# Kernel tuning notes

Hardware: AMD Instinct MI355X
Metric: run time of the kernel (lower is better)

## Reference

```python
import jax, jax.numpy as jnp
import numpy as np

H = 8      # heads
D = 64     # dim_head
DIM = 512  # model dim (== H*D)
LN_EPS = 1e-5


def setup_inputs() -> dict:
    key = jax.random.key(0)
    ks = jax.random.split(key, 4)
    B, N = 8, 1024
    x = jax.random.normal(ks[0], (B, N, DIM), dtype=jnp.float32)
    # params (torch Linear y = x @ W^T; we store W already transposed as (in, out))
    w_qkv = jax.random.normal(ks[1], (DIM, 3 * H * D), dtype=jnp.float32) * (DIM ** -0.5)
    w_out = jax.random.normal(ks[2], (H * D, DIM), dtype=jnp.float32) * ((H * D) ** -0.5)
    b_out = jnp.zeros((DIM,), dtype=jnp.float32)
    ln_g = jnp.ones((DIM,), dtype=jnp.float32)
    ln_b = jnp.zeros((DIM,), dtype=jnp.float32)
    return {"x": x, "w_qkv": w_qkv, "w_out": w_out, "b_out": b_out,
            "ln_g": ln_g, "ln_b": ln_b}


def reference(x, w_qkv, w_out, b_out, ln_g, ln_b):
    b, n, _ = x.shape
    qkv = x @ w_qkv                                   # [b, n, 3*H*D]
    q, k, v = jnp.split(qkv, 3, axis=-1)              # each [b, n, H*D]

    def to_heads(t):                                  # 'b n (h d) -> (b h) n d'
        return t.reshape(b, n, H, D).transpose(0, 2, 1, 3).reshape(b * H, n, D)

    q = to_heads(q)
    k = to_heads(k)
    v = to_heads(v)

    # FAITHFUL to source: k.view(b*h, -1, n) is a row-major reshape, NOT a
    # transpose, and NO scale is applied (self.scale is unused in forward).
    k_r = k.reshape(b * H, D, n)                      # [(bh), D, n] reinterpreted
    dots = jnp.matmul(q, k_r)                          # [(bh), n, n]
    attn = jax.nn.softmax(dots, axis=-1)
    out = jnp.matmul(attn, v)                          # [(bh), n, D]

    # '(b h) n d -> b n (h d)'
    out = out.reshape(b, H, n, D).transpose(0, 2, 1, 3).reshape(b, n, H * D)
    out = out @ w_out + b_out                          # to_out Linear (dropout=0)

    mu = jnp.mean(out, axis=-1, keepdims=True)
    var = jnp.var(out, axis=-1, keepdims=True)
    out = (out - mu) * jax.lax.rsqrt(var + LN_EPS) * ln_g + ln_b
    return out + x
```

## Files before the change

kernel.cpp:

```cpp
#include <hip/hip_runtime.h>

typedef unsigned short u16;
typedef unsigned int u32;
typedef __attribute__((ext_vector_type(4))) float f32x4;
typedef __attribute__((ext_vector_type(8))) short s16x8;
typedef __attribute__((ext_vector_type(4))) unsigned int u32x4;

__device__ __forceinline__ u16 bf16_rne(float f) {
    u32 u = __float_as_uint(f);
    u32 r = u + 0x7FFFu + ((u >> 16) & 1u);
    return (u16)(r >> 16);
}

__device__ __forceinline__ u32 cvt_pk_bf16(float lo, float hi) {
    u32 r;
    asm("v_cvt_pk_bf16_f32 %0, %1, %2" : "=v"(r) : "v"(lo), "v"(hi));
    return r;
}

__device__ __forceinline__ void gl_lds16(const void* g, void* l) {
    __builtin_amdgcn_global_load_lds(
        (const __attribute__((address_space(1))) u32*)g,
        (__attribute__((address_space(3))) u32*)l, 16, 0, 0);
}

#define MFMA16(a, b, c) __builtin_amdgcn_mfma_f32_16x16x32_bf16((a), (b), (c), 0, 0, 0)

__global__ __launch_bounds__(256) void k_transpose2(const float* __restrict__ w_qkv,
                                                    const float* __restrict__ w_out,
                                                    u16* __restrict__ wqkvt,
                                                    u16* __restrict__ woutt) {
    __shared__ float tile[32][33];
    const float* in;
    u16* out;
    int C, bxc;
    if (blockIdx.x < 48) { in = w_qkv; out = wqkvt; C = 1536; bxc = blockIdx.x; }
    else                 { in = w_out; out = woutt; C = 512;  bxc = blockIdx.x - 48; }
    const int R = 512;
    int bx = bxc * 32;
    int by = blockIdx.y * 32;
    int tx = threadIdx.x;
    int ty = threadIdx.y;
#pragma unroll
    for (int i = 0; i < 32; i += 8)
        tile[ty + i][tx] = in[(size_t)(by + ty + i) * C + bx + tx];
    __syncthreads();
#pragma unroll
    for (int i = 0; i < 32; i += 8)
        out[(size_t)(bx + ty + i) * R + by + tx] = bf16_rne(tile[tx][ty + i]);
}

__global__ __launch_bounds__(256) void k_qkv_gemm(
    const float* __restrict__ x, const u16* __restrict__ wt,
    u16* __restrict__ qh, u16* __restrict__ kRT, u16* __restrict__ vT) {
    __shared__ __align__(16) u16 lA[2][128 * 64];
    __shared__ __align__(16) u16 lB[2][128 * 64];
    const int tid = threadIdx.x;
    const int lane = tid & 63, l15 = lane & 15, l4 = lane >> 4;
    const int wid = tid >> 6, wm = wid >> 1, wn = wid & 1;
    const int m0 = blockIdx.y * 128;
    const int c0 = blockIdx.x * 128;

    const char* gX = (const char*)x + (size_t)m0 * 2048;
    const char* gB = (const char*)wt + (size_t)c0 * 1024;
    const int srow = tid >> 3;
    const int cc = tid & 7;
    const int scol = cc * 16;

    const f32x4 z4 = {0.f, 0.f, 0.f, 0.f};
    f32x4 acc[4][4];
#pragma unroll
    for (int i = 0; i < 4; ++i)
#pragma unroll
        for (int j = 0; j < 4; ++j) acc[i][j] = z4;

    f32x4 ax[4][2];
    auto loadA = [&](int kt) {
#pragma unroll
        for (int q = 0; q < 4; ++q) {
            const char* src = gX + (size_t)(q * 32 + srow) * 2048 + kt * 256 + cc * 32;
            ax[q][0] = *(const f32x4*)(src);
            ax[q][1] = *(const f32x4*)(src + 16);
        }
    };
    auto writeA = [&](int buf) {
#pragma unroll
        for (int q = 0; q < 4; ++q) {
            int row = q * 32 + srow;
            u32x4 v;
            v.x = cvt_pk_bf16(ax[q][0].x, ax[q][0].y);
            v.y = cvt_pk_bf16(ax[q][0].z, ax[q][0].w);
            v.z = cvt_pk_bf16(ax[q][1].x, ax[q][1].y);
            v.w = cvt_pk_bf16(ax[q][1].z, ax[q][1].w);
            *(u32x4*)((char*)lA[buf] + row * 128 + (scol ^ ((row & 7) << 4))) = v;
        }
    };
    auto stageB = [&](int buf, int kt) {
#pragma unroll
        for (int q = 0; q < 4; ++q) {
            int row = q * 32 + srow;
            int sc = scol ^ ((row & 7) << 4);
            gl_lds16(gB + (size_t)row * 1024 + kt * 128 + sc,
                     (char*)lB[buf] + q * 4096 + tid * 16);
        }
    };

    loadA(0);
    stageB(0, 0);
    writeA(0);
    __syncthreads();
    for (int kt = 0; kt < 8; ++kt) {
        int buf = kt & 1;
        if (kt < 7) {
            loadA(kt + 1);
            stageB(buf ^ 1, kt + 1);
        }
        s16x8 af[4][2], bfr[4][2];
#pragma unroll
        for (int i = 0; i < 4; ++i)
#pragma unroll
            for (int k2 = 0; k2 < 2; ++k2) {
                int ra = wm * 64 + i * 16 + l15;
                int ca = (k2 * 64 + l4 * 16) ^ ((ra & 7) << 4);
                af[i][k2] = *(const s16x8*)((const char*)lA[buf] + ra * 128 + ca);
                int rb = wn * 64 + i * 16 + l15;
                int cb = (k2 * 64 + l4 * 16) ^ ((rb & 7) << 4);
                bfr[i][k2] = *(const s16x8*)((const char*)lB[buf] + rb * 128 + cb);
            }
        __builtin_amdgcn_s_setprio(1);
#pragma unroll
        for (int i = 0; i < 4; ++i)
#pragma unroll
            for (int j = 0; j < 4; ++j)
#pragma unroll
                for (int k2 = 0; k2 < 2; ++k2)
                    acc[i][j] = MFMA16(af[i][k2], bfr[j][k2], acc[i][j]);
        __builtin_amdgcn_s_setprio(0);
        if (kt < 7) writeA(buf ^ 1);
        __syncthreads();
    }

    char* ct = (char*)lA;
    const int which = c0 >> 9;
    const int hb = (c0 & 511) >> 6;
    const int b = m0 >> 10;
    const int n0 = m0 & 1023;
    const int i4 = (m0 >> 7) & 7;

    if (which != 2) {
#pragma unroll
        for (int i = 0; i < 4; ++i)
#pragma unroll
            for (int j = 0; j < 4; ++j) {
                int col = wn * 64 + j * 16 + l15;
#pragma unroll
                for (int r = 0; r < 4; ++r) {
                    int rr = wm * 64 + i * 16 + l4 * 4 + r;
                    *(u16*)(ct + rr * 256 + ((col * 2) ^ ((rr & 7) << 4))) =
                        bf16_rne(acc[i][j][r]);
                }
            }
    } else {
#pragma unroll
        for (int i = 0; i < 4; ++i)
#pragma unroll
            for (int j = 0; j < 4; ++j) {
                int col = wn * 64 + j * 16 + l15;
#pragma unroll
                for (int r = 0; r < 4; ++r) {
                    int rr = wm * 64 + i * 16 + l4 * 4 + r;
                    *(u16*)(ct + col * 256 + ((rr * 2) ^ ((col & 7) << 4))) =
                        bf16_rne(acc[i][j][r]);
                }
            }
    }
    __syncthreads();

    if (which == 0) {
#pragma unroll
        for (int p = 0; p < 8; ++p) {
            int cid = p * 256 + tid;
            int row = cid >> 4, sub = cid & 15;
            s16x8 v = *(const s16x8*)(ct + row * 256 + ((sub * 16) ^ ((row & 7) << 4)));
            int bh = b * 8 + hb + (sub >> 3);
            *(s16x8*)((char*)qh + ((size_t)bh * 1024 + n0 + row) * 128 +
                      (sub & 7) * 16) = v;
        }
    } else if (which == 1) {
#pragma unroll
        for (int p = 0; p < 8; ++p) {
            int cid = p * 256 + tid;
            int h = cid >> 10, jb = (cid >> 6) & 15, jd = cid & 63;
            int colb = ((h * 64 + jd) * 2) ^ ((jb & 7) << 4);
            s16x8 v;
#pragma unroll
            for (int ii = 0; ii < 8; ++ii)
                v[ii] = *(const short*)(ct + (jb + ii * 16) * 256 + colb);
            int bh = b * 8 + hb + h;
            *(s16x8*)((char*)kRT + (size_t)bh * 131072 + jb * 8192 + i4 * 1024 +
                      jd * 16) = v;
        }
    } else {
#pragma unroll
        for (int p = 0; p < 8; ++p) {
            int cid = p * 256 + tid;
            int cl = cid >> 4, nc = cid & 15;
            s16x8 v = *(const s16x8*)(ct + cl * 256 + ((nc * 16) ^ ((cl & 7) << 4)));
            int bh = b * 8 + hb + (cl >> 6);
            *(s16x8*)((char*)vT + ((size_t)bh * 64 + (cl & 63)) * 2048 + n0 * 2 +
                      nc * 16) = v;
        }
    }
}

__global__ __launch_bounds__(512) void k_attn(
    const u16* __restrict__ qh, const u16* __restrict__ kRT,
    const u16* __restrict__ vT, u16* __restrict__ attn_out) {
    __shared__ __align__(16) char smem[49152];
    char* qtile = smem;
    char* ktb = smem + 16384;
    char* vtb = smem + 32768;

    const int tid = threadIdx.x;
    const int lane = tid & 63, l15 = lane & 15, l4 = lane >> 4;
    const int wid = tid >> 6;
    const int bh = blockIdx.x, mt = blockIdx.y;

    const char* kb = (const char*)kRT + (size_t)bh * 131072;
    const char* vb = (const char*)vT + (size_t)bh * 64 * 2048;
    const int srow = tid >> 3;
    const int scol = (tid & 7) * 16;

    {
        const char* gq = (const char*)qh + ((size_t)bh * 1024 + mt * 128) * 128;
#pragma unroll
        for (int q = 0; q < 2; ++q) {
            int row = q * 64 + srow;
            int sc = scol ^ ((row & 7) << 4);
            gl_lds16(gq + (size_t)row * 128 + sc, qtile + q * 8192 + tid * 16);
        }
        int i4s = (tid & 7) ^ (srow & 7);
        gl_lds16(kb + i4s * 1024 + srow * 16, ktb + tid * 16);
        int sc = scol ^ ((srow & 7) << 4);
        gl_lds16(vb + (size_t)srow * 2048 + sc, vtb + tid * 16);
    }
    __syncthreads();

    s16x8 qf[2];
#pragma unroll
    for (int k2 = 0; k2 < 2; ++k2) {
        int row = wid * 16 + l15;
        int cq = (k2 * 64 + l4 * 16) ^ ((row & 7) << 4);
        qf[k2] = *(const s16x8*)(qtile + row * 128 + cq);
    }
    __syncthreads();

    char* ptw = smem + wid * 2048;

    const f32x4 z4 = {0.f, 0.f, 0.f, 0.f};
    f32x4 o[4];
    float den = 0.f;
#pragma unroll
    for (int d4 = 0; d4 < 4; ++d4) o[d4] = z4;
    const float LOG2E = 1.4426950408889634f;

    for (int jb = 0; jb < 16; ++jb) {
        const int buf = jb & 1;
        if (jb < 15) {
            int nb = jb + 1, bufn = buf ^ 1;
            int i4s = (tid & 7) ^ (srow & 7);
            gl_lds16(kb + (size_t)nb * 8192 + i4s * 1024 + srow * 16,
                     ktb + bufn * 8192 + tid * 16);
            int sc = scol ^ ((srow & 7) << 4);
            gl_lds16(vb + (size_t)srow * 2048 + nb * 128 + sc,
                     vtb + bufn * 8192 + tid * 16);
        }
        const char* kt = ktb + buf * 8192;
        const char* vt = vtb + buf * 8192;

        s16x8 bk[4][2];
#pragma unroll
        for (int n4 = 0; n4 < 4; ++n4)
#pragma unroll
            for (int k2 = 0; k2 < 2; ++k2) {
                int rn = n4 * 16 + l15;
                int cb = (k2 * 64 + l4 * 16) ^ ((rn & 7) << 4);
                bk[n4][k2] = *(const s16x8*)(kt + rn * 128 + cb);
            }
        f32x4 s[4];
        __builtin_amdgcn_s_setprio(1);
#pragma unroll
        for (int n4 = 0; n4 < 4; ++n4) {
            s[n4] = z4;
#pragma unroll
            for (int k2 = 0; k2 < 2; ++k2)
                s[n4] = MFMA16(bk[n4][k2], qf[k2], s[n4]);
        }
        __builtin_amdgcn_s_setprio(0);

#pragma unroll
        for (int n4 = 0; n4 < 4; ++n4) {
            float e0 = exp2f(s[n4][0] * LOG2E);
            float e1 = exp2f(s[n4][1] * LOG2E);
            float e2 = exp2f(s[n4][2] * LOG2E);
            float e3 = exp2f(s[n4][3] * LOG2E);
            den += (e0 + e1) + (e2 + e3);
            uint2 w;
            w.x = cvt_pk_bf16(e0, e1);
            w.y = cvt_pk_bf16(e2, e3);
            *(uint2*)(ptw + l15 * 128 +
                      ((n4 * 32 + l4 * 8) ^ ((l15 & 7) << 4))) = w;
        }

        s16x8 bv[4][2];
#pragma unroll
        for (int d4 = 0; d4 < 4; ++d4)
#pragma unroll
            for (int k2 = 0; k2 < 2; ++k2) {
                int rn = d4 * 16 + l15;
                int cb = (k2 * 64 + l4 * 16) ^ ((rn & 7) << 4);
                bv[d4][k2] = *(const s16x8*)(vt + rn * 128 + cb);
            }

        s16x8 pa[2];
#pragma unroll
        for (int k2 = 0; k2 < 2; ++k2)
            pa[k2] = *(const s16x8*)(ptw + l15 * 128 +
                                     ((k2 * 64 + l4 * 16) ^ ((l15 & 7) << 4)));

        __builtin_amdgcn_s_setprio(1);
#pragma unroll
        for (int d4 = 0; d4 < 4; ++d4)
#pragma unroll
            for (int k2 = 0; k2 < 2; ++k2)
                o[d4] = MFMA16(bv[d4][k2], pa[k2], o[d4]);
        __builtin_amdgcn_s_setprio(0);

        if (jb < 15) __syncthreads();
    }

    den += __shfl_xor(den, 16);
    den += __shfl_xor(den, 32);
    float inv = 1.0f / den;

    {
        int row = wid * 16 + l15;
        char* ow = smem + row * 128;
#pragma unroll
        for (int d4 = 0; d4 < 4; ++d4) {
            uint2 w;
            w.x = cvt_pk_bf16(o[d4][0] * inv, o[d4][1] * inv);
            w.y = cvt_pk_bf16(o[d4][2] * inv, o[d4][3] * inv);
            *(uint2*)(ow + ((d4 * 32 + l4 * 8) ^ ((row & 7) << 4))) = w;
        }
    }
    __syncthreads();

    {
        char* dst = (char*)attn_out + ((size_t)(bh >> 3) * 1024 + mt * 128) * 1024 +
                    (bh & 7) * 128;
#pragma unroll
        for (int p = 0; p < 2; ++p) {
            int cid = p * 512 + tid;
            int row = cid >> 3, sub = cid & 7;
            s16x8 v = *(const s16x8*)(smem + row * 128 +
                                      ((sub * 16) ^ ((row & 7) << 4)));
            *(s16x8*)(dst + (size_t)row * 1024 + sub * 16) = v;
        }
    }
}

__global__ __launch_bounds__(512) void k_out_ln(
    const u16* __restrict__ aout, const u16* __restrict__ wt,
    const float* __restrict__ bias, const float* __restrict__ x,
    const float* __restrict__ g, const float* __restrict__ bb,
    float* __restrict__ out) {
    __shared__ __align__(16) char smem[131072];
    char* lB[2] = {smem, smem + 65536};
    const int tid = threadIdx.x;
    const int lane = tid & 63, l15 = lane & 15, l4 = lane >> 4;
    const int wid = tid >> 6, wm = wid >> 2, wn = wid & 3;
    const int m0 = blockIdx.x * 32;

    s16x8 af[16];
    {
        const char* arow = (const char*)aout + (size_t)(m0 + wm * 16 + l15) * 1024;
#pragma unroll
        for (int kk = 0; kk < 16; ++kk)
            af[kk] = *(const s16x8*)(arow + kk * 64 + l4 * 16);
    }

    auto stageB = [&](int buf, int kt) {
#pragma unroll
        for (int p = 0; p < 8; ++p) {
            int cid = p * 512 + tid;
            int n = cid >> 3, cc = cid & 7;
            int sc = (cc * 16) ^ ((n & 7) << 4);
            gl_lds16((const char*)wt + (size_t)n * 1024 + kt * 128 + sc,
                     lB[buf] + cid * 16);
        }
    };

    const f32x4 z4 = {0.f, 0.f, 0.f, 0.f};
    f32x4 acc[8];
#pragma unroll
    for (int j = 0; j < 8; ++j) acc[j] = z4;

    stageB(0, 0);
    __syncthreads();
    for (int kt = 0; kt < 8; ++kt) {
        int buf = kt & 1;
        if (kt < 7) stageB(buf ^ 1, kt + 1);
        s16x8 bf2[8][2];
#pragma unroll
        for (int j = 0; j < 8; ++j)
#pragma unroll
            for (int q = 0; q < 2; ++q) {
                int n = wn * 128 + j * 16 + l15;
                int cb = (q * 64 + l4 * 16) ^ ((n & 7) << 4);
                bf2[j][q] = *(const s16x8*)(lB[buf] + n * 128 + cb);
            }
        __builtin_amdgcn_s_setprio(1);
#pragma unroll
        for (int j = 0; j < 8; ++j)
#pragma unroll
            for (int q = 0; q < 2; ++q)
                acc[j] = MFMA16(af[kt * 2 + q], bf2[j][q], acc[j]);
        __builtin_amdgcn_s_setprio(0);
        __syncthreads();
    }

#pragma unroll
    for (int j = 0; j < 8; ++j) {
        int col = wn * 128 + j * 16 + l15;
        float bo = bias[col];
#pragma unroll
        for (int r = 0; r < 4; ++r) {
            int row = wm * 16 + l4 * 4 + r;
            *(float*)(smem + row * 2048 + ((col * 4) ^ ((row & 7) << 4))) =
                acc[j][r] + bo;
        }
    }
    __syncthreads();

    f32x4 g0 = *(const f32x4*)(g + lane * 8);
    f32x4 g1 = *(const f32x4*)(g + lane * 8 + 4);
    f32x4 b0 = *(const f32x4*)(bb + lane * 8);
    f32x4 b1 = *(const f32x4*)(bb + lane * 8 + 4);
#pragma unroll
    for (int rr = 0; rr < 4; ++rr) {
        int row = wid * 4 + rr;
        int sw = (row & 7) << 4;
        f32x4 v0 = *(const f32x4*)(smem + row * 2048 + ((lane * 32) ^ sw));
        f32x4 v1 = *(const f32x4*)(smem + row * 2048 + ((lane * 32 + 16) ^ sw));
        float s = v0.x + v0.y + v0.z + v0.w + v1.x + v1.y + v1.z + v1.w;
        float sq = v0.x * v0.x + v0.y * v0.y + v0.z * v0.z + v0.w * v0.w +
                   v1.x * v1.x + v1.y * v1.y + v1.z * v1.z + v1.w * v1.w;
#pragma unroll
        for (int m = 1; m < 64; m <<= 1) {
            s += __shfl_xor(s, m);
            sq += __shfl_xor(sq, m);
        }
        float mu = s * (1.0f / 512.0f);
        float var = sq * (1.0f / 512.0f) - mu * mu;
        float rstd = rsqrtf(var + 1e-5f);

        const float* xr = x + (size_t)(m0 + row) * 512 + lane * 8;
        f32x4 x0 = *(const f32x4*)(xr);
        f32x4 x1 = *(const f32x4*)(xr + 4);
        f32x4 r0, r1;
#pragma unroll
        for (int u = 0; u < 4; ++u) {
            r0[u] = (v0[u] - mu) * rstd * g0[u] + b0[u] + x0[u];
            r1[u] = (v1[u] - mu) * rstd * g1[u] + b1[u] + x1[u];
        }
        float* orow = out + (size_t)(m0 + row) * 512 + lane * 8;
        *(f32x4*)(orow) = r0;
        *(f32x4*)(orow + 4) = r1;
    }
}

extern "C" void kernel_launch(void* const* d_in, const int* in_sizes, int n_in,
                              void* d_out, int out_size, void* d_ws, size_t ws_size,
                              hipStream_t stream) {
    const float* x = (const float*)d_in[0];
    const float* w_qkv = (const float*)d_in[1];
    const float* w_out = (const float*)d_in[2];
    const float* b_out = (const float*)d_in[3];
    const float* ln_g = (const float*)d_in[4];
    const float* ln_b = (const float*)d_in[5];
    float* out = (float*)d_out;
    char* ws = (char*)d_ws;

    u16* wqkvt = (u16*)(ws + 0);
    u16* woutt = (u16*)(ws + 1572864);
    u16* qh = (u16*)(ws + 2097152);
    u16* kRT = (u16*)(ws + 10485760);
    u16* vT = (u16*)(ws + 18874368);
    u16* aout = (u16*)(ws + 27262976);

    k_transpose2<<<dim3(64, 16), dim3(32, 8), 0, stream>>>(w_qkv, w_out, wqkvt, woutt);
    k_qkv_gemm<<<dim3(12, 64), 256, 0, stream>>>(x, wqkvt, qh, kRT, vT);
    k_attn<<<dim3(64, 8), 512, 0, stream>>>(qh, kRT, vT, aout);
    k_out_ln<<<256, 512, 0, stream>>>(aout, woutt, b_out, x, ln_g, ln_b, out);
}
```

Measured before the change: 87.46 us.

## Pre-convert x to bf16 and stage A via direct global-to-LDS loads with block swizzle

Adds a separate kernel that converts x from fp32 to bf16 once. The QKV GEMM can then stage its A operand through global_load_lds the same way as B, instead of loading fp32 into registers, converting, and writing to LDS. This removes the register pressure and the VALU conversion work inside the GEMM main loop, and it stops each of the 12 column tiles from re-reading and re-converting fp32 x. The GEMM grid also changes to a 1D launch with a block remapping meant to improve L2 locality across blocks. The cost is an extra kernel launch plus an 8 MB bf16 write and read, which also enlarges the workspace.

```diff
diff --git a/kernel.cpp b/kernel.cpp
--- a/kernel.cpp
+++ b/kernel.cpp
@@ -4,7 +4,6 @@
 typedef unsigned int u32;
 typedef __attribute__((ext_vector_type(4))) float f32x4;
 typedef __attribute__((ext_vector_type(8))) short s16x8;
-typedef __attribute__((ext_vector_type(4))) unsigned int u32x4;
 
 __device__ __forceinline__ u16 bf16_rne(float f) {
     u32 u = __float_as_uint(f);
@@ -25,6 +24,18 @@
 }
 
 #define MFMA16(a, b, c) __builtin_amdgcn_mfma_f32_16x16x32_bf16((a), (b), (c), 0, 0, 0)
+
+__global__ __launch_bounds__(256) void k_convert(const float* __restrict__ in,
+                                                 u16* __restrict__ out, int n4) {
+    int i = blockIdx.x * 256 + threadIdx.x;
+    if (i >= n4) return;
+    f32x4 v = *(const f32x4*)(in + (size_t)i * 4);
+    u32 lo = cvt_pk_bf16(v.x, v.y);
+    u32 hi = cvt_pk_bf16(v.z, v.w);
+    u32* p = (u32*)(out + (size_t)i * 4);
+    p[0] = lo;
+    p[1] = hi;
+}
 
 __global__ __launch_bounds__(256) void k_transpose2(const float* __restrict__ w_qkv,
                                                     const float* __restrict__ w_out,
@@ -51,21 +62,22 @@
 }
 
 __global__ __launch_bounds__(256) void k_qkv_gemm(
-    const float* __restrict__ x, const u16* __restrict__ wt,
+    const u16* __restrict__ xbf, const u16* __restrict__ wt,
     u16* __restrict__ qh, u16* __restrict__ kRT, u16* __restrict__ vT) {
     __shared__ __align__(16) u16 lA[2][128 * 64];
     __shared__ __align__(16) u16 lB[2][128 * 64];
     const int tid = threadIdx.x;
     const int lane = tid & 63, l15 = lane & 15, l4 = lane >> 4;
     const int wid = tid >> 6, wm = wid >> 1, wn = wid & 1;
-    const int m0 = blockIdx.y * 128;
-    const int c0 = blockIdx.x * 128;
-
-    const char* gX = (const char*)x + (size_t)m0 * 2048;
+    const int hw = blockIdx.x;
+    const int e = hw & 7, idx = hw >> 3;
+    const int m0 = (e + 8 * (idx / 12)) * 128;
+    const int c0 = (idx % 12) * 128;
+
+    const char* gA = (const char*)xbf + (size_t)m0 * 1024;
     const char* gB = (const char*)wt + (size_t)c0 * 1024;
     const int srow = tid >> 3;
-    const int cc = tid & 7;
-    const int scol = cc * 16;
+    const int scol = (tid & 7) * 16;
 
     const f32x4 z4 = {0.f, 0.f, 0.f, 0.f};
     f32x4 acc[4][4];
@@ -74,47 +86,23 @@
 #pragma unroll
         for (int j = 0; j < 4; ++j) acc[i][j] = z4;
 
-    f32x4 ax[4][2];
-    auto loadA = [&](int kt) {
-#pragma unroll
-        for (int q = 0; q < 4; ++q) {
-            const char* src = gX + (size_t)(q * 32 + srow) * 2048 + kt * 256 + cc * 32;
-            ax[q][0] = *(const f32x4*)(src);
-            ax[q][1] = *(const f32x4*)(src + 16);
-        }
-    };
-    auto writeA = [&](int buf) {
-#pragma unroll
-        for (int q = 0; q < 4; ++q) {
-            int row = q * 32 + srow;
-            u32x4 v;
-            v.x = cvt_pk_bf16(ax[q][0].x, ax[q][0].y);
-            v.y = cvt_pk_bf16(ax[q][0].z, ax[q][0].w);
-            v.z = cvt_pk_bf16(ax[q][1].x, ax[q][1].y);
-            v.w = cvt_pk_bf16(ax[q][1].z, ax[q][1].w);
-            *(u32x4*)((char*)lA[buf] + row * 128 + (scol ^ ((row & 7) << 4))) = v;
-        }
-    };
-    auto stageB = [&](int buf, int kt) {
+    auto stage = [&](int buf, int kt) {
 #pragma unroll
         for (int q = 0; q < 4; ++q) {
             int row = q * 32 + srow;
             int sc = scol ^ ((row & 7) << 4);
+            gl_lds16(gA + (size_t)row * 1024 + kt * 128 + sc,
+                     (char*)lA[buf] + q * 4096 + tid * 16);
             gl_lds16(gB + (size_t)row * 1024 + kt * 128 + sc,
                      (char*)lB[buf] + q * 4096 + tid * 16);
         }
     };
 
-    loadA(0);
-    stageB(0, 0);
-    writeA(0);
+    stage(0, 0);
     __syncthreads();
     for (int kt = 0; kt < 8; ++kt) {
         int buf = kt & 1;
-        if (kt < 7) {
-            loadA(kt + 1);
-            stageB(buf ^ 1, kt + 1);
-        }
+        if (kt < 7) stage(buf ^ 1, kt + 1);
         s16x8 af[4][2], bfr[4][2];
 #pragma unroll
         for (int i = 0; i < 4; ++i)
@@ -136,7 +124,6 @@
                 for (int k2 = 0; k2 < 2; ++k2)
                     acc[i][j] = MFMA16(af[i][k2], bfr[j][k2], acc[i][j]);
         __builtin_amdgcn_s_setprio(0);
-        if (kt < 7) writeA(buf ^ 1);
         __syncthreads();
     }
 
@@ -492,15 +479,17 @@
     float* out = (float*)d_out;
     char* ws = (char*)d_ws;
 
-    u16* wqkvt = (u16*)(ws + 0);
-    u16* woutt = (u16*)(ws + 1572864);
-    u16* qh = (u16*)(ws + 2097152);
-    u16* kRT = (u16*)(ws + 10485760);
-    u16* vT = (u16*)(ws + 18874368);
-    u16* aout = (u16*)(ws + 27262976);
-
+    u16* xbf = (u16*)(ws + 0);
+    u16* wqkvt = (u16*)(ws + 8388608);
+    u16* woutt = (u16*)(ws + 9961472);
+    u16* qh = (u16*)(ws + 10485760);
+    u16* kRT = (u16*)(ws + 18874368);
+    u16* vT = (u16*)(ws + 27262976);
+    u16* aout = (u16*)(ws + 35651584);
+
+    k_convert<<<4096, 256, 0, stream>>>(x, xbf, 1048576);
     k_transpose2<<<dim3(64, 16), dim3(32, 8), 0, stream>>>(w_qkv, w_out, wqkvt, woutt);
-    k_qkv_gemm<<<dim3(12, 64), 256, 0, stream>>>(x, wqkvt, qh, kRT, vT);
+    k_qkv_gemm<<<768, 256, 0, stream>>>(xbf, wqkvt, qh, kRT, vT);
     k_attn<<<dim3(64, 8), 512, 0, stream>>>(qh, kRT, vT, aout);
     k_out_ln<<<256, 512, 0, stream>>>(aout, woutt, b_out, x, ln_g, ln_b, out);
 }
```

Result: faster. 81.12 us (-7.3%).
